# Kernel optimization log

Measured on AMD Instinct MI355X. Metric: run time of the kernel, lower is better.

The kernel has to match this reference:

```python
import jax, jax.numpy as jnp
import numpy as np

VOCAB = 256; EMB = 384; D_MODEL = 512; D_INNER = 1024; D_STATE = 16
D_CONV = 4; DT_RANK = 32; NL = 8; B = 2; L = 2048

def silu(x):
    return x * jax.nn.sigmoid(x)

def layernorm(x, g, b):
    mu = x.mean(-1, keepdims=True)
    v = ((x - mu) ** 2).mean(-1, keepdims=True)
    return (x - mu) / jnp.sqrt(v + 1e-5) * g + b

def conv1d_same(x, w, b, pad):
    # x: (B, C, L), w: (O, I, K)
    out = jax.lax.conv_general_dilated(x, w, (1,), [(pad, pad)],
                                       dimension_numbers=('NCH', 'OIH', 'NCH'))
    return out + b[None, :, None]

def mamba_layer(x, in_w, cw, cb, xp_w, dt_w, dt_b, A_log, Dp, out_w):
    # x: (B, L, D_MODEL)
    xz = x @ in_w.T                      # (B, L, 2*D_INNER)
    xi, z = xz[..., :D_INNER], xz[..., D_INNER:]
    # causal depthwise conv over time
    xi_t = xi.transpose(0, 2, 1)         # (B, D_INNER, L)
    xc = jax.lax.conv_general_dilated(xi_t, cw[:, None, :], (1,), [(D_CONV - 1, 0)],
                                      dimension_numbers=('NCH', 'OIH', 'NCH'),
                                      feature_group_count=D_INNER)
    xc = silu(xc + cb[None, :, None]).transpose(0, 2, 1)   # (B, L, D_INNER)
    dbc = xc @ xp_w.T                    # (B, L, DT_RANK + 2*D_STATE)
    dt = jax.nn.softplus(dbc[..., :DT_RANK] @ dt_w.T + dt_b)   # (B, L, D_INNER)
    Bm = dbc[..., DT_RANK:DT_RANK + D_STATE]                    # (B, L, D_STATE)
    Cm = dbc[..., DT_RANK + D_STATE:]                           # (B, L, D_STATE)
    A = -jnp.exp(A_log)                                         # (D_INNER, D_STATE)
    dA = jnp.exp(dt[..., None] * A)                             # (B, L, D_INNER, D_STATE)
    dBx = (dt * xc)[..., None] * Bm[:, :, None, :]              # (B, L, D_INNER, D_STATE)

    def step(h, inp):
        a, bx, c = inp
        h = a * h + bx                                          # (B, D_INNER, D_STATE)
        return h, jnp.einsum('bds,bs->bd', h, c)

    h0 = jnp.zeros((x.shape[0], D_INNER, D_STATE), x.dtype)
    _, ys = jax.lax.scan(step, h0, (dA.transpose(1, 0, 2, 3),
                                    dBx.transpose(1, 0, 2, 3),
                                    Cm.transpose(1, 0, 2)))
    y = ys.transpose(1, 0, 2) + Dp * xc                         # (B, L, D_INNER)
    y = y * silu(z)
    return y @ out_w.T

def setup_inputs() -> dict:
    key = jax.random.key(0)
    ks = jax.random.split(key, 24)
    s = 0.02
    inp = {
        'tokens': jax.random.randint(ks[0], (B, L), 0, VOCAB),
        'emb': jax.random.normal(ks[1], (VOCAB, EMB)) * s,
        'conv1_w': jax.random.normal(ks[2], (512, EMB, 5)) * s,
        'conv1_b': jnp.zeros((512,)),
        'ln1_g': jnp.ones((512,)), 'ln1_b': jnp.zeros((512,)),
        'conv2_w': jax.random.normal(ks[3], (512, 512, 3)) * s,
        'conv2_b': jnp.zeros((512,)),
        'ln2_g': jnp.ones((512,)), 'ln2_b': jnp.zeros((512,)),
        'pos_emb': jax.random.normal(ks[4], (L, D_MODEL)) * s,
        'in_proj_w': jax.random.normal(ks[5], (NL, 2 * D_INNER, D_MODEL)) * s,
        'conv_w': jax.random.normal(ks[6], (NL, D_INNER, D_CONV)) * s,
        'conv_b': jnp.zeros((NL, D_INNER)),
        'x_proj_w': jax.random.normal(ks[7], (NL, DT_RANK + 2 * D_STATE, D_INNER)) * s,
        'dt_proj_w': jax.random.normal(ks[8], (NL, D_INNER, DT_RANK)) * s,
        'dt_proj_b': jnp.full((NL, D_INNER), -4.0),
        'A_log': jnp.log(jnp.tile(jnp.arange(1, D_STATE + 1, dtype=jnp.float32),
                                  (NL, D_INNER, 1))),
        'D': jnp.ones((NL, D_INNER)),
        'out_proj_w': jax.random.normal(ks[9], (NL, D_MODEL, D_INNER)) * s,
        'fc_w': jax.random.normal(ks[10], (VOCAB, D_MODEL)) * s,
        'fc_b': jnp.zeros((VOCAB,)),
    }
    return inp

def reference(tokens, emb, conv1_w, conv1_b, ln1_g, ln1_b, conv2_w, conv2_b,
              ln2_g, ln2_b, pos_emb, in_proj_w, conv_w, conv_b, x_proj_w,
              dt_proj_w, dt_proj_b, A_log, D, out_proj_w, fc_w, fc_b):
    x = emb[tokens]                                   # (B, L, EMB)
    # CNN frontend (GELU + channel LayerNorm, dropout=0 in eval)
    x = x.transpose(0, 2, 1)
    x = jax.nn.gelu(conv1d_same(x, conv1_w, conv1_b, 2), approximate=False)
    x = layernorm(x.transpose(0, 2, 1), ln1_g, ln1_b).transpose(0, 2, 1)
    x = jax.nn.gelu(conv1d_same(x, conv2_w, conv2_b, 1), approximate=False)
    x = layernorm(x.transpose(0, 2, 1), ln2_g, ln2_b)  # (B, L, 512)
    x = x + pos_emb[None, :x.shape[1]]
    for i in range(NL):
        x = mamba_layer(x, in_proj_w[i], conv_w[i], conv_b[i], x_proj_w[i],
                        dt_proj_w[i], dt_proj_b[i], A_log[i], D[i], out_proj_w[i])
    rep = x[:, -1, :]
    return rep @ fc_w.T + fc_b
```

## Files before the change

kernel.cpp:

```cpp
#include <hip/hip_runtime.h>
#include <hip/hip_bf16.h>
#include <math.h>

#define VOCABN 256
#define EMBN   384
#define DM     512
#define DI     1024
#define DSTATE 16
#define DCONVN 4
#define DTRANK 32
#define NLAYER 8
#define BBATCH 2
#define LSEQ   2048
#define MROWS  (BBATCH*LSEQ)
#define SCHUNK 32
#define NCHUNK (LSEQ/SCHUNK)

typedef short s8v  __attribute__((ext_vector_type(8)));
typedef float f32x4 __attribute__((ext_vector_type(4)));

__device__ __forceinline__ ushort f2bf(float f) {
    uint u = __float_as_uint(f);
    return (ushort)((u + 0x7fffu + ((u >> 16) & 1u)) >> 16);
}
__device__ __forceinline__ float bf2f(ushort h) {
    return __uint_as_float((uint)h << 16);
}
__device__ __forceinline__ uint packbf(float f) {
    ushort h = f2bf(f);
    ushort l = f2bf(f - bf2f(h));
    return ((uint)h << 16) | (uint)l;
}
__device__ __forceinline__ void unp4(uint4 p, ushort* hdst, ushort* ldst) {
    ushort4 h, l;
    h.x = (ushort)(p.x >> 16); l.x = (ushort)(p.x & 0xffffu);
    h.y = (ushort)(p.y >> 16); l.y = (ushort)(p.y & 0xffffu);
    h.z = (ushort)(p.z >> 16); l.z = (ushort)(p.z & 0xffffu);
    h.w = (ushort)(p.w >> 16); l.w = (ushort)(p.w & 0xffffu);
    *(ushort4*)hdst = h; *(ushort4*)ldst = l;
}

__global__ void pack4_kernel(const float* __restrict__ a, int na,
                             const float* __restrict__ b, int nb,
                             const float* __restrict__ c, int nc,
                             const float* __restrict__ d, int nd,
                             uint* __restrict__ pa, uint* __restrict__ pb,
                             uint* __restrict__ pc, uint* __restrict__ pd) {
    int i = blockIdx.x * 256 + threadIdx.x;
    if (i < na) pa[i] = packbf(a[i]);
    else if (i < na + nb) pb[i - na] = packbf(b[i - na]);
    else if (i < na + nb + nc) pc[i - na - nb] = packbf(c[i - na - nb]);
    else if (i < na + nb + nc + nd) pd[i - na - nb - nc] = packbf(d[i - na - nb - nc]);
}

template<int CI, int CK>
__global__ void pack_convw_kernel(const float* __restrict__ w, uint* __restrict__ pw) {
    int idx = blockIdx.x * 256 + threadIdx.x;
    if (idx >= 512 * CI * CK) return;
    int k  = idx % CK;
    int ci = (idx / CK) % CI;
    int co = idx / (CK * CI);
    pw[((size_t)(k * 512) + co) * CI + ci] = packbf(w[idx]);
}

__global__ void embed_kernel(const int* __restrict__ tok, const float* __restrict__ emb,
                             uint* __restrict__ px0) {
    int idx = blockIdx.x * 256 + threadIdx.x;
    int c = idx % EMBN;
    int t = idx / EMBN;
    px0[idx] = packbf(emb[tok[t] * EMBN + c]);
}

__device__ __forceinline__ float gelu_exact(float x) {
    return 0.5f * x * (1.f + erff(x * 0.70710678118654752f));
}

template<int CI, int CK, int PAD>
__global__ __launch_bounds__(256) void conv_mfma_kernel(
    const uint* __restrict__ PA, const uint* __restrict__ PW,
    const float* __restrict__ bias, float* __restrict__ out)
{
    constexpr int ROWS = 64 + CK - 1;
    const int t0  = blockIdx.x * 64;
    const int co0 = blockIdx.y * 32;
    const int tid = threadIdx.x;
    const int wid = tid >> 6, lane = tid & 63;
    const int rb = (wid >> 1) * 32;
    const int cb = (wid & 1) * 16;
    const int lr = lane & 15, lk = (lane >> 4) * 8;
    const int bstart = (t0 / LSEQ) * LSEQ;

    __shared__ alignas(16) ushort Ah[ROWS][40], Al[ROWS][40];
    __shared__ alignas(16) ushort Bh[CK][32][40], Bl[CK][32][40];

    f32x4 acc[2];
#pragma unroll
    for (int m = 0; m < 2; m++) acc[m] = (f32x4){0.f, 0.f, 0.f, 0.f};

    for (int ci0 = 0; ci0 < CI; ci0 += 32) {
        __syncthreads();
        for (int idx = tid; idx < ROWS * 8; idx += 256) {
            int r = idx >> 3, c4 = (idx & 7) * 4;
            int g = t0 - PAD + r;
            uint4 v = make_uint4(0u, 0u, 0u, 0u);
            if (g >= bstart && g < bstart + LSEQ)
                v = *(const uint4*)&PA[(size_t)g * CI + ci0 + c4];
            unp4(v, &Ah[r][c4], &Al[r][c4]);
        }
        for (int idx = tid; idx < CK * 32 * 8; idx += 256) {
            int k = idx >> 8;
            int r = (idx >> 3) & 31;
            int c4 = (idx & 7) * 4;
            uint4 v = *(const uint4*)&PW[((size_t)(k * 512) + co0 + r) * CI + ci0 + c4];
            unp4(v, &Bh[k][r][c4], &Bl[k][r][c4]);
        }
        __syncthreads();

#pragma unroll
        for (int k = 0; k < CK; k++) {
            s8v ah[2], al[2], bh, bl;
#pragma unroll
            for (int m = 0; m < 2; m++) {
                ah[m] = *(const s8v*)&Ah[rb + m * 16 + lr + k][lk];
                al[m] = *(const s8v*)&Al[rb + m * 16 + lr + k][lk];
            }
            bh = *(const s8v*)&Bh[k][cb + lr][lk];
            bl = *(const s8v*)&Bl[k][cb + lr][lk];
#pragma unroll
            for (int m = 0; m < 2; m++) {
                acc[m] = __builtin_amdgcn_mfma_f32_16x16x32_bf16(ah[m], bh, acc[m], 0, 0, 0);
                acc[m] = __builtin_amdgcn_mfma_f32_16x16x32_bf16(ah[m], bl, acc[m], 0, 0, 0);
                acc[m] = __builtin_amdgcn_mfma_f32_16x16x32_bf16(al[m], bh, acc[m], 0, 0, 0);
            }
        }
    }

    int gcol = co0 + cb + lr;
    float bv = bias[gcol];
#pragma unroll
    for (int m = 0; m < 2; m++) {
#pragma unroll
        for (int r = 0; r < 4; r++) {
            int grow = t0 + rb + m * 16 + (lane >> 4) * 4 + r;
            out[(size_t)grow * 512 + gcol] = gelu_exact(acc[m][r] + bv);
        }
    }
}

template<bool ADDPOS, bool PACK>
__global__ __launch_bounds__(256) void ln_kernel(
    const float* __restrict__ in, const float* __restrict__ g, const float* __restrict__ bb,
    const float* __restrict__ pos, float* __restrict__ out, uint* __restrict__ pout)
{
    int row  = blockIdx.x * 4 + (threadIdx.x >> 6);
    int lane = threadIdx.x & 63;
    const float* xr = in + (size_t)row * DM;
    float v[8];
    float s = 0.f;
#pragma unroll
    for (int i = 0; i < 8; i++) { v[i] = xr[lane + i * 64]; s += v[i]; }
#pragma unroll
    for (int o = 32; o >= 1; o >>= 1) s += __shfl_xor(s, o);
    float mu = s * (1.f / 512.f);
    float var = 0.f;
#pragma unroll
    for (int i = 0; i < 8; i++) { float d = v[i] - mu; var = fmaf(d, d, var); }
#pragma unroll
    for (int o = 32; o >= 1; o >>= 1) var += __shfl_xor(var, o);
    var *= (1.f / 512.f);
    float rstd = rsqrtf(var + 1e-5f);
    int t = row & (LSEQ - 1);
#pragma unroll
    for (int i = 0; i < 8; i++) {
        int c = lane + i * 64;
        float o = (v[i] - mu) * rstd * g[c] + bb[c];
        if (ADDPOS) o += pos[t * DM + c];
        if (PACK) pout[(size_t)row * DM + c] = packbf(o);
        else      out [(size_t)row * DM + c] = o;
    }
}

template<int BM, int BN, int WM, int WN, int EPI>
__global__ __launch_bounds__(256) void gemm_mfma_p(
    const uint* __restrict__ PA, int lda,
    const uint* __restrict__ PW,
    const float* __restrict__ bias,
    float* __restrict__ C, uint* __restrict__ PC, int N, int K)
{
    constexpr int MR = BM / WM / 16;
    constexpr int NR = BN / WN / 16;
    constexpr int NLOAD = (BM + BN) * 8 / 256;
    const int m0 = blockIdx.x * BM;
    const int n0 = blockIdx.y * BN;
    const int tid = threadIdx.x;
    const int wid = tid >> 6;
    const int lane = tid & 63;
    const int rb = (wid / WN) * (BM / WM);
    const int cb = (wid % WN) * (BN / WN);
    const int lr = lane & 15;
    const int lk = (lane >> 4) * 8;

    __shared__ alignas(16) ushort Ah[BM][40], Al[BM][40];
    __shared__ alignas(16) ushort Bh[BN][40], Bl[BN][40];

    f32x4 acc[MR][NR];
#pragma unroll
    for (int m = 0; m < MR; m++)
#pragma unroll
        for (int n = 0; n < NR; n++) acc[m][n] = (f32x4){0.f, 0.f, 0.f, 0.f};

    for (int k0 = 0; k0 < K; k0 += 32) {
        uint4 v[NLOAD];
#pragma unroll
        for (int i = 0; i < NLOAD; i++) {
            int idx = tid + i * 256;
            int row = idx >> 3, c4 = (idx & 7) * 4;
            v[i] = (row < BM)
                 ? *(const uint4*)&PA[(size_t)(m0 + row) * lda + k0 + c4]
                 : *(const uint4*)&PW[(size_t)(n0 + row - BM) * K + k0 + c4];
        }
        __syncthreads();
#pragma unroll
        for (int i = 0; i < NLOAD; i++) {
            int idx = tid + i * 256;
            int row = idx >> 3, c4 = (idx & 7) * 4;
            if (row < BM) unp4(v[i], &Ah[row][c4], &Al[row][c4]);
            else          unp4(v[i], &Bh[row - BM][c4], &Bl[row - BM][c4]);
        }
        __syncthreads();

        s8v ah[MR], al[MR], bh[NR], bl[NR];
#pragma unroll
        for (int m = 0; m < MR; m++) {
            ah[m] = *(const s8v*)&Ah[rb + m * 16 + lr][lk];
            al[m] = *(const s8v*)&Al[rb + m * 16 + lr][lk];
        }
#pragma unroll
        for (int n = 0; n < NR; n++) {
            bh[n] = *(const s8v*)&Bh[cb + n * 16 + lr][lk];
            bl[n] = *(const s8v*)&Bl[cb + n * 16 + lr][lk];
        }
#pragma unroll
        for (int m = 0; m < MR; m++)
#pragma unroll
            for (int n = 0; n < NR; n++) {
                acc[m][n] = __builtin_amdgcn_mfma_f32_16x16x32_bf16(ah[m], bh[n], acc[m][n], 0, 0, 0);
                acc[m][n] = __builtin_amdgcn_mfma_f32_16x16x32_bf16(ah[m], bl[n], acc[m][n], 0, 0, 0);
                acc[m][n] = __builtin_amdgcn_mfma_f32_16x16x32_bf16(al[m], bh[n], acc[m][n], 0, 0, 0);
            }
    }

#pragma unroll
    for (int m = 0; m < MR; m++)
#pragma unroll
        for (int n = 0; n < NR; n++) {
#pragma unroll
            for (int r = 0; r < 4; r++) {
                int grow = m0 + rb + m * 16 + (lane >> 4) * 4 + r;
                int gcol = n0 + cb + n * 16 + lr;
                float v = acc[m][n][r];
                if (EPI == 3) {
                    v += bias[gcol];
                    v = fmaxf(v, 0.f) + log1pf(expf(-fabsf(v)));
                }
                C[(size_t)grow * N + gcol] = v;
                if (EPI == 2) PC[(size_t)grow * N + gcol] = packbf(v);
            }
        }
}

__global__ void dwconv_silu_kernel(const float* __restrict__ xz, const float* __restrict__ cw,
                                   const float* __restrict__ cb, float* __restrict__ xc,
                                   uint* __restrict__ pxc) {
    int idx = blockIdx.x * 256 + threadIdx.x;
    int d = idx & (DI - 1);
    int r = idx >> 10;
    int tl = r & (LSEQ - 1);
    float acc = cb[d];
#pragma unroll
    for (int k = 0; k < DCONVN; k++) {
        int ts = tl - 3 + k;
        if (ts >= 0) acc = fmaf(xz[(size_t)(r - 3 + k) * (2 * DI) + d], cw[d * DCONVN + k], acc);
    }
    float sig = 1.f / (1.f + expf(-acc));
    float v = acc * sig;
    xc[idx] = v;
    pxc[idx] = packbf(v);
}

__global__ __launch_bounds__(256) void scan_local_kernel(
    const float* __restrict__ dt, const float* __restrict__ xc,
    const float* __restrict__ dbc, const float* __restrict__ A_log,
    float* __restrict__ S, float* __restrict__ P)
{
    const int sg = threadIdx.x & 3;
    const int dl = threadIdx.x >> 2;
    const int dq = blockIdx.x & 15;
    const int c  = (blockIdx.x >> 4) & (NCHUNK - 1);
    const int b  = blockIdx.x / (16 * NCHUNK);
    const int d  = dq * 64 + dl;

    float4 alog = *(const float4*)&A_log[d * DSTATE + sg * 4];
    float Av[4];
    Av[0] = -expf(alog.x) * 1.44269504f;
    Av[1] = -expf(alog.y) * 1.44269504f;
    Av[2] = -expf(alog.z) * 1.44269504f;
    Av[3] = -expf(alog.w) * 1.44269504f;

    float h[4] = {0.f, 0.f, 0.f, 0.f};
    float sumdt = 0.f;
    const int rowbase = b * LSEQ + c * SCHUNK;

#pragma unroll 4
    for (int t = 0; t < SCHUNK; t++) {
        int r = rowbase + t;
        float dtv = dt[(size_t)r * DI + d];
        float xcv = xc[(size_t)r * DI + d];
        float4 Bv = *(const float4*)&dbc[(size_t)r * 64 + DTRANK + sg * 4];
        float dx = dtv * xcv;
        h[0] = fmaf(exp2f(dtv * Av[0]), h[0], dx * Bv.x);
        h[1] = fmaf(exp2f(dtv * Av[1]), h[1], dx * Bv.y);
        h[2] = fmaf(exp2f(dtv * Av[2]), h[2], dx * Bv.z);
        h[3] = fmaf(exp2f(dtv * Av[3]), h[3], dx * Bv.w);
        sumdt += dtv;
    }
    size_t off = ((size_t)(b * NCHUNK + c) * DI + d) * DSTATE + sg * 4;
    *(float4*)&S[off] = make_float4(h[0], h[1], h[2], h[3]);
    *(float4*)&P[off] = make_float4(exp2f(Av[0] * sumdt), exp2f(Av[1] * sumdt),
                                    exp2f(Av[2] * sumdt), exp2f(Av[3] * sumdt));
}

__global__ __launch_bounds__(256) void scan_combine_kernel(
    const float* __restrict__ S, const float* __restrict__ P, float* __restrict__ H)
{
    int idx = blockIdx.x * 256 + threadIdx.x;
    int b = idx >> 14;
    int rem = idx & 16383;
    float h = 0.f;
#pragma unroll
    for (int c = 0; c < NCHUNK; c++) {
        size_t off = ((size_t)(b * NCHUNK + c) * DI) * DSTATE + rem;
        H[off] = h;
        h = fmaf(P[off], h, S[off]);
    }
}

__global__ __launch_bounds__(256) void scan_out_kernel(
    const float* __restrict__ dt, const float* __restrict__ xc,
    const float* __restrict__ dbc, const float* __restrict__ xz,
    const float* __restrict__ A_log, const float* __restrict__ Dp,
    const float* __restrict__ H, uint* __restrict__ py)
{
    const int sg = threadIdx.x & 3;
    const int dl = threadIdx.x >> 2;
    const int dq = blockIdx.x & 15;
    const int c  = (blockIdx.x >> 4) & (NCHUNK - 1);
    const int b  = blockIdx.x / (16 * NCHUNK);
    const int d  = dq * 64 + dl;

    float4 alog = *(const float4*)&A_log[d * DSTATE + sg * 4];
    float Av[4];
    Av[0] = -expf(alog.x) * 1.44269504f;
    Av[1] = -expf(alog.y) * 1.44269504f;
    Av[2] = -expf(alog.z) * 1.44269504f;
    Av[3] = -expf(alog.w) * 1.44269504f;
    float Dval = Dp[d];

    float4 hv = *(const float4*)&H[((size_t)(b * NCHUNK + c) * DI + d) * DSTATE + sg * 4];
    float h[4] = {hv.x, hv.y, hv.z, hv.w};
    const int rowbase = b * LSEQ + c * SCHUNK;

#pragma unroll 2
    for (int t = 0; t < SCHUNK; t++) {
        int r = rowbase + t;
        float dtv = dt[(size_t)r * DI + d];
        float xcv = xc[(size_t)r * DI + d];
        float4 Bv = *(const float4*)&dbc[(size_t)r * 64 + DTRANK + sg * 4];
        float4 Cv = *(const float4*)&dbc[(size_t)r * 64 + DTRANK + DSTATE + sg * 4];
        float dx = dtv * xcv;
        h[0] = fmaf(exp2f(dtv * Av[0]), h[0], dx * Bv.x);
        h[1] = fmaf(exp2f(dtv * Av[1]), h[1], dx * Bv.y);
        h[2] = fmaf(exp2f(dtv * Av[2]), h[2], dx * Bv.z);
        h[3] = fmaf(exp2f(dtv * Av[3]), h[3], dx * Bv.w);
        float p = h[0] * Cv.x;
        p = fmaf(h[1], Cv.y, p);
        p = fmaf(h[2], Cv.z, p);
        p = fmaf(h[3], Cv.w, p);
        p += __shfl_xor(p, 1);
        p += __shfl_xor(p, 2);
        if (sg == 0) {
            float zv = xz[(size_t)r * (2 * DI) + DI + d];
            float zsig = 1.f / (1.f + exp2f(-zv * 1.44269504f));
            py[(size_t)r * DI + d] = packbf((p + Dval * xcv) * (zv * zsig));
        }
    }
}

__global__ void fc_kernel(const float* __restrict__ x, const float* __restrict__ fcw,
                          const float* __restrict__ fcb, float* __restrict__ out) {
    int b = blockIdx.x;
    int v = threadIdx.x;
    __shared__ float rep[DM];
    const float* xr = x + (size_t)(b * LSEQ + LSEQ - 1) * DM;
    for (int i = threadIdx.x; i < DM; i += 256) rep[i] = xr[i];
    __syncthreads();
    float acc = fcb[v];
    for (int k = 0; k < DM; k++) acc = fmaf(rep[k], fcw[v * DM + k], acc);
    out[b * VOCABN + v] = acc;
}

extern "C" void kernel_launch(void* const* d_in, const int* in_sizes, int n_in,
                              void* d_out, int out_size, void* d_ws, size_t ws_size,
                              hipStream_t stream) {
    const int*   tokens    = (const int*)  d_in[0];
    const float* emb       = (const float*)d_in[1];
    const float* conv1_w   = (const float*)d_in[2];
    const float* conv1_b   = (const float*)d_in[3];
    const float* ln1_g     = (const float*)d_in[4];
    const float* ln1_b     = (const float*)d_in[5];
    const float* conv2_w   = (const float*)d_in[6];
    const float* conv2_b   = (const float*)d_in[7];
    const float* ln2_g     = (const float*)d_in[8];
    const float* ln2_b     = (const float*)d_in[9];
    const float* pos_emb   = (const float*)d_in[10];
    const float* in_proj_w = (const float*)d_in[11];
    const float* conv_w    = (const float*)d_in[12];
    const float* conv_b    = (const float*)d_in[13];
    const float* x_proj_w  = (const float*)d_in[14];
    const float* dt_proj_w = (const float*)d_in[15];
    const float* dt_proj_b = (const float*)d_in[16];
    const float* A_log     = (const float*)d_in[17];
    const float* Dp_all    = (const float*)d_in[18];
    const float* out_proj_w= (const float*)d_in[19];
    const float* fc_w      = (const float*)d_in[20];
    const float* fc_b      = (const float*)d_in[21];

    float* ws = (float*)d_ws;
    float* X    = ws;
    float* T1   = X   + 2097152;
    float* XZ   = T1  + 2097152;
    float* XC   = XZ  + 8388608;
    float* DT   = XC  + 4194304;
    uint*  PY   = (uint*)(DT + 4194304);
    float* DBC  = (float*)PY + 4194304;
    uint*  PX   = (uint*)(DBC + 262144);
    uint*  PXC  = PX  + 2097152;
    uint*  PWIN = PXC + 4194304;
    uint*  PWOUT= PWIN + 1048576;
    uint*  PWX  = PWOUT + 524288;
    uint*  PWDT = PWX + 65536;
    uint*  PDBC = PWDT + 32768;
    uint*  PX0  = (uint*)XZ;
    uint*  PWC1 = (uint*)XC;
    uint*  PWC2 = (uint*)XC + 983040;
    uint*  PB   = (uint*)DT;
    float* SCN_S = T1;
    float* SCN_P = (float*)PXC;
    float* SCN_H = (float*)PXC + 2097152;

    pack_convw_kernel<EMBN, 5><<<(512 * EMBN * 5 + 255) / 256, 256, 0, stream>>>(conv1_w, PWC1);
    pack_convw_kernel<DM,   3><<<(512 * DM   * 3 + 255) / 256, 256, 0, stream>>>(conv2_w, PWC2);
    embed_kernel<<<(MROWS * EMBN) / 256, 256, 0, stream>>>(tokens, emb, PX0);
    conv_mfma_kernel<EMBN, 5, 2><<<dim3(MROWS / 64, 16), 256, 0, stream>>>(PX0, PWC1, conv1_b, T1);
    ln_kernel<false, true><<<MROWS / 4, 256, 0, stream>>>(T1, ln1_g, ln1_b, nullptr, nullptr, PB);
    conv_mfma_kernel<DM, 3, 1><<<dim3(MROWS / 64, 16), 256, 0, stream>>>(PB, PWC2, conv2_b, T1);
    ln_kernel<true, true><<<MROWS / 4, 256, 0, stream>>>(T1, ln2_g, ln2_b, pos_emb, nullptr, PX);

    const int NPACK = 2 * DI * DM + DM * DI + 64 * DI + DI * DTRANK;
    for (int l = 0; l < NLAYER; l++) {
        pack4_kernel<<<(NPACK + 255) / 256, 256, 0, stream>>>(
            in_proj_w + (size_t)l * 2 * DI * DM, 2 * DI * DM,
            out_proj_w + (size_t)l * DM * DI, DM * DI,
            x_proj_w + (size_t)l * 64 * DI, 64 * DI,
            dt_proj_w + (size_t)l * DI * DTRANK, DI * DTRANK,
            PWIN, PWOUT, PWX, PWDT);
        gemm_mfma_p<64, 128, 1, 4, 0><<<dim3(MROWS / 64, (2 * DI) / 128), 256, 0, stream>>>(
            PX, DM, PWIN, nullptr, XZ, nullptr, 2 * DI, DM);
        dwconv_silu_kernel<<<(MROWS * DI) / 256, 256, 0, stream>>>(
            XZ, conv_w + (size_t)l * DI * DCONVN, conv_b + (size_t)l * DI, XC, PXC);
        gemm_mfma_p<64, 64, 2, 2, 2><<<dim3(MROWS / 64, 1), 256, 0, stream>>>(
            PXC, DI, PWX, nullptr, DBC, PDBC, 64, DI);
        gemm_mfma_p<64, 64, 2, 2, 3><<<dim3(MROWS / 64, DI / 64), 256, 0, stream>>>(
            PDBC, 64, PWDT, dt_proj_b + (size_t)l * DI, DT, nullptr, DI, DTRANK);
        scan_local_kernel<<<16 * NCHUNK * BBATCH, 256, 0, stream>>>(
            DT, XC, DBC, A_log + (size_t)l * DI * DSTATE, SCN_S, SCN_P);
        scan_combine_kernel<<<(BBATCH * DI * DSTATE) / 256, 256, 0, stream>>>(
            SCN_S, SCN_P, SCN_H);
        scan_out_kernel<<<16 * NCHUNK * BBATCH, 256, 0, stream>>>(
            DT, XC, DBC, XZ, A_log + (size_t)l * DI * DSTATE, Dp_all + (size_t)l * DI,
            SCN_H, PY);
        gemm_mfma_p<64, 64, 2, 2, 2><<<dim3(MROWS / 64, DM / 64), 256, 0, stream>>>(
            PY, DI, PWOUT, nullptr, X, PX, DM, DI);
    }

    fc_kernel<<<BBATCH, 256, 0, stream>>>(X, fc_w, fc_b, (float*)d_out);
}
```

Before: 1.868 ms.

## Restructure chunked scan: compute local outputs in first pass, apply state correction elementwise

The two sequential per-chunk scan passes become one. The forward pass now computes the chunk-local output and the cumulative dt in the same loop that produces the chunk end-states. A new elementwise kernel then adds the carried-in state contribution using exp(A*cumdt)*H*C and applies the z gate. A_log is turned into A*log2e once inside the packing kernel, so the scan kernels no longer call exp on it. This removes a second sequential recurrence over each chunk, at the cost of extra fp32 round trips through memory and 16 exp2 calls per output element in the correction kernel.

New measurement: 1.924 ms. 1.03x slower.

```diff
diff --git a/kernel.cpp b/kernel.cpp
--- a/kernel.cpp
+++ b/kernel.cpp
@@ -40,17 +40,23 @@
     *(ushort4*)hdst = h; *(ushort4*)ldst = l;
 }
 
-__global__ void pack4_kernel(const float* __restrict__ a, int na,
+__global__ void pack5_kernel(const float* __restrict__ a, int na,
                              const float* __restrict__ b, int nb,
                              const float* __restrict__ c, int nc,
                              const float* __restrict__ d, int nd,
+                             const float* __restrict__ alog, int ne,
                              uint* __restrict__ pa, uint* __restrict__ pb,
-                             uint* __restrict__ pc, uint* __restrict__ pd) {
+                             uint* __restrict__ pc, uint* __restrict__ pd,
+                             float* __restrict__ av) {
     int i = blockIdx.x * 256 + threadIdx.x;
     if (i < na) pa[i] = packbf(a[i]);
     else if (i < na + nb) pb[i - na] = packbf(b[i - na]);
     else if (i < na + nb + nc) pc[i - na - nb] = packbf(c[i - na - nb]);
     else if (i < na + nb + nc + nd) pd[i - na - nb - nc] = packbf(d[i - na - nb - nc]);
+    else if (i < na + nb + nc + nd + ne) {
+        int j = i - na - nb - nc - nd;
+        av[j] = -expf(alog[j]) * 1.44269504f;
+    }
 }
 
 template<int CI, int CK>
@@ -263,8 +269,10 @@
                     v += bias[gcol];
                     v = fmaxf(v, 0.f) + log1pf(expf(-fabsf(v)));
                 }
-                C[(size_t)grow * N + gcol] = v;
-                if (EPI == 2) PC[(size_t)grow * N + gcol] = packbf(v);
+                if (EPI == 0 || EPI == 2 || EPI == 3)
+                    C[(size_t)grow * N + gcol] = v;
+                if (EPI == 2)
+                    PC[(size_t)grow * N + gcol] = packbf(v);
             }
         }
 }
@@ -288,10 +296,14 @@
     pxc[idx] = packbf(v);
 }
 
-__global__ __launch_bounds__(256) void scan_local_kernel(
-    const float* __restrict__ dt, const float* __restrict__ xc,
-    const float* __restrict__ dbc, const float* __restrict__ A_log,
-    float* __restrict__ S, float* __restrict__ P)
+__global__ __launch_bounds__(256) void scan_fwd_kernel(
+    float* dtbuf,
+    const float* __restrict__ xc,
+    const float* __restrict__ dbc,
+    const float* __restrict__ AV,
+    const float* __restrict__ Dp,
+    float* __restrict__ S, float* __restrict__ P,
+    float* __restrict__ ylocal)
 {
     const int sg = threadIdx.x & 3;
     const int dl = threadIdx.x >> 2;
@@ -300,83 +312,22 @@
     const int b  = blockIdx.x / (16 * NCHUNK);
     const int d  = dq * 64 + dl;
 
-    float4 alog = *(const float4*)&A_log[d * DSTATE + sg * 4];
-    float Av[4];
-    Av[0] = -expf(alog.x) * 1.44269504f;
-    Av[1] = -expf(alog.y) * 1.44269504f;
-    Av[2] = -expf(alog.z) * 1.44269504f;
-    Av[3] = -expf(alog.w) * 1.44269504f;
+    float4 av = *(const float4*)&AV[d * DSTATE + sg * 4];
+    float Av[4] = {av.x, av.y, av.z, av.w};
+    float Dval = Dp[d];
 
     float h[4] = {0.f, 0.f, 0.f, 0.f};
     float sumdt = 0.f;
     const int rowbase = b * LSEQ + c * SCHUNK;
 
-#pragma unroll 4
-    for (int t = 0; t < SCHUNK; t++) {
-        int r = rowbase + t;
-        float dtv = dt[(size_t)r * DI + d];
-        float xcv = xc[(size_t)r * DI + d];
-        float4 Bv = *(const float4*)&dbc[(size_t)r * 64 + DTRANK + sg * 4];
-        float dx = dtv * xcv;
-        h[0] = fmaf(exp2f(dtv * Av[0]), h[0], dx * Bv.x);
-        h[1] = fmaf(exp2f(dtv * Av[1]), h[1], dx * Bv.y);
-        h[2] = fmaf(exp2f(dtv * Av[2]), h[2], dx * Bv.z);
-        h[3] = fmaf(exp2f(dtv * Av[3]), h[3], dx * Bv.w);
-        sumdt += dtv;
-    }
-    size_t off = ((size_t)(b * NCHUNK + c) * DI + d) * DSTATE + sg * 4;
-    *(float4*)&S[off] = make_float4(h[0], h[1], h[2], h[3]);
-    *(float4*)&P[off] = make_float4(exp2f(Av[0] * sumdt), exp2f(Av[1] * sumdt),
-                                    exp2f(Av[2] * sumdt), exp2f(Av[3] * sumdt));
-}
-
-__global__ __launch_bounds__(256) void scan_combine_kernel(
-    const float* __restrict__ S, const float* __restrict__ P, float* __restrict__ H)
-{
-    int idx = blockIdx.x * 256 + threadIdx.x;
-    int b = idx >> 14;
-    int rem = idx & 16383;
-    float h = 0.f;
-#pragma unroll
-    for (int c = 0; c < NCHUNK; c++) {
-        size_t off = ((size_t)(b * NCHUNK + c) * DI) * DSTATE + rem;
-        H[off] = h;
-        h = fmaf(P[off], h, S[off]);
-    }
-}
-
-__global__ __launch_bounds__(256) void scan_out_kernel(
-    const float* __restrict__ dt, const float* __restrict__ xc,
-    const float* __restrict__ dbc, const float* __restrict__ xz,
-    const float* __restrict__ A_log, const float* __restrict__ Dp,
-    const float* __restrict__ H, uint* __restrict__ py)
-{
-    const int sg = threadIdx.x & 3;
-    const int dl = threadIdx.x >> 2;
-    const int dq = blockIdx.x & 15;
-    const int c  = (blockIdx.x >> 4) & (NCHUNK - 1);
-    const int b  = blockIdx.x / (16 * NCHUNK);
-    const int d  = dq * 64 + dl;
-
-    float4 alog = *(const float4*)&A_log[d * DSTATE + sg * 4];
-    float Av[4];
-    Av[0] = -expf(alog.x) * 1.44269504f;
-    Av[1] = -expf(alog.y) * 1.44269504f;
-    Av[2] = -expf(alog.z) * 1.44269504f;
-    Av[3] = -expf(alog.w) * 1.44269504f;
-    float Dval = Dp[d];
-
-    float4 hv = *(const float4*)&H[((size_t)(b * NCHUNK + c) * DI + d) * DSTATE + sg * 4];
-    float h[4] = {hv.x, hv.y, hv.z, hv.w};
-    const int rowbase = b * LSEQ + c * SCHUNK;
-
 #pragma unroll 2
     for (int t = 0; t < SCHUNK; t++) {
-        int r = rowbase + t;
-        float dtv = dt[(size_t)r * DI + d];
-        float xcv = xc[(size_t)r * DI + d];
-        float4 Bv = *(const float4*)&dbc[(size_t)r * 64 + DTRANK + sg * 4];
-        float4 Cv = *(const float4*)&dbc[(size_t)r * 64 + DTRANK + DSTATE + sg * 4];
+        size_t off = (size_t)(rowbase + t) * DI + d;
+        float dtv = dtbuf[off];
+        float xcv = xc[off];
+        float4 Bv = *(const float4*)&dbc[(size_t)(rowbase + t) * 64 + DTRANK + sg * 4];
+        float4 Cv = *(const float4*)&dbc[(size_t)(rowbase + t) * 64 + DTRANK + DSTATE + sg * 4];
+        sumdt += dtv;
         float dx = dtv * xcv;
         h[0] = fmaf(exp2f(dtv * Av[0]), h[0], dx * Bv.x);
         h[1] = fmaf(exp2f(dtv * Av[1]), h[1], dx * Bv.y);
@@ -389,11 +340,66 @@
         p += __shfl_xor(p, 1);
         p += __shfl_xor(p, 2);
         if (sg == 0) {
-            float zv = xz[(size_t)r * (2 * DI) + DI + d];
-            float zsig = 1.f / (1.f + exp2f(-zv * 1.44269504f));
-            py[(size_t)r * DI + d] = packbf((p + Dval * xcv) * (zv * zsig));
-        }
-    }
+            ylocal[off] = p + Dval * xcv;
+            dtbuf[off] = sumdt;
+        }
+    }
+    size_t soff = ((size_t)(b * NCHUNK + c) * DI + d) * DSTATE + sg * 4;
+    *(float4*)&S[soff] = make_float4(h[0], h[1], h[2], h[3]);
+    *(float4*)&P[soff] = make_float4(exp2f(Av[0] * sumdt), exp2f(Av[1] * sumdt),
+                                     exp2f(Av[2] * sumdt), exp2f(Av[3] * sumdt));
+}
+
+__global__ __launch_bounds__(256) void scan_combine_kernel(
+    const float* __restrict__ S, const float* __restrict__ P, float* __restrict__ H)
+{
+    int idx = blockIdx.x * 256 + threadIdx.x;
+    int b = idx >> 14;
+    int rem = idx & 16383;
+    float h = 0.f;
+#pragma unroll
+    for (int c = 0; c < NCHUNK; c++) {
+        size_t off = ((size_t)(b * NCHUNK + c) * DI) * DSTATE + rem;
+        H[off] = h;
+        h = fmaf(P[off], h, S[off]);
+    }
+}
+
+__global__ __launch_bounds__(256) void scan_corr_kernel(
+    const float* __restrict__ cumdt,
+    const float* __restrict__ dbc,
+    const float* __restrict__ xz,
+    const float* __restrict__ AV,
+    const float* __restrict__ H,
+    uint* __restrict__ py)
+{
+    int idx = blockIdx.x * 256 + threadIdx.x;
+    int d = idx & (DI - 1);
+    int r = idx >> 10;
+    int t = r & (LSEQ - 1);
+    int b = r >> 11;
+    int c = t / SCHUNK;
+
+    float cd = cumdt[idx];
+    float yl = __uint_as_float(py[idx]);
+    float zv = xz[(size_t)r * (2 * DI) + DI + d];
+    const float* Hp = &H[((size_t)(b * NCHUNK + c) * DI + d) * DSTATE];
+    const float* Cp = &dbc[(size_t)r * 64 + DTRANK + DSTATE];
+    const float* Ap = &AV[d * DSTATE];
+
+    float corr = 0.f;
+#pragma unroll
+    for (int s = 0; s < DSTATE; s += 4) {
+        float4 Hv = *(const float4*)&Hp[s];
+        float4 Cv = *(const float4*)&Cp[s];
+        float4 Avv = *(const float4*)&Ap[s];
+        corr = fmaf(Cv.x * exp2f(Avv.x * cd), Hv.x, corr);
+        corr = fmaf(Cv.y * exp2f(Avv.y * cd), Hv.y, corr);
+        corr = fmaf(Cv.z * exp2f(Avv.z * cd), Hv.z, corr);
+        corr = fmaf(Cv.w * exp2f(Avv.w * cd), Hv.w, corr);
+    }
+    float zsig = 1.f / (1.f + exp2f(-zv * 1.44269504f));
+    py[idx] = packbf((yl + corr) * (zv * zsig));
 }
 
 __global__ void fc_kernel(const float* __restrict__ x, const float* __restrict__ fcw,
@@ -450,6 +456,7 @@
     uint*  PWX  = PWOUT + 524288;
     uint*  PWDT = PWX + 65536;
     uint*  PDBC = PWDT + 32768;
+    float* AVB  = (float*)(PDBC + 262144);
     uint*  PX0  = (uint*)XZ;
     uint*  PWC1 = (uint*)XC;
     uint*  PWC2 = (uint*)XC + 983040;
@@ -466,14 +473,15 @@
     conv_mfma_kernel<DM, 3, 1><<<dim3(MROWS / 64, 16), 256, 0, stream>>>(PB, PWC2, conv2_b, T1);
     ln_kernel<true, true><<<MROWS / 4, 256, 0, stream>>>(T1, ln2_g, ln2_b, pos_emb, nullptr, PX);
 
-    const int NPACK = 2 * DI * DM + DM * DI + 64 * DI + DI * DTRANK;
+    const int NPACK = 2 * DI * DM + DM * DI + 64 * DI + DI * DTRANK + DI * DSTATE;
     for (int l = 0; l < NLAYER; l++) {
-        pack4_kernel<<<(NPACK + 255) / 256, 256, 0, stream>>>(
+        pack5_kernel<<<(NPACK + 255) / 256, 256, 0, stream>>>(
             in_proj_w + (size_t)l * 2 * DI * DM, 2 * DI * DM,
             out_proj_w + (size_t)l * DM * DI, DM * DI,
             x_proj_w + (size_t)l * 64 * DI, 64 * DI,
             dt_proj_w + (size_t)l * DI * DTRANK, DI * DTRANK,
-            PWIN, PWOUT, PWX, PWDT);
+            A_log + (size_t)l * DI * DSTATE, DI * DSTATE,
+            PWIN, PWOUT, PWX, PWDT, AVB);
         gemm_mfma_p<64, 128, 1, 4, 0><<<dim3(MROWS / 64, (2 * DI) / 128), 256, 0, stream>>>(
             PX, DM, PWIN, nullptr, XZ, nullptr, 2 * DI, DM);
         dwconv_silu_kernel<<<(MROWS * DI) / 256, 256, 0, stream>>>(
@@ -482,13 +490,12 @@
             PXC, DI, PWX, nullptr, DBC, PDBC, 64, DI);
         gemm_mfma_p<64, 64, 2, 2, 3><<<dim3(MROWS / 64, DI / 64), 256, 0, stream>>>(
             PDBC, 64, PWDT, dt_proj_b + (size_t)l * DI, DT, nullptr, DI, DTRANK);
-        scan_local_kernel<<<16 * NCHUNK * BBATCH, 256, 0, stream>>>(
-            DT, XC, DBC, A_log + (size_t)l * DI * DSTATE, SCN_S, SCN_P);
+        scan_fwd_kernel<<<16 * NCHUNK * BBATCH, 256, 0, stream>>>(
+            DT, XC, DBC, AVB, Dp_all + (size_t)l * DI, SCN_S, SCN_P, (float*)PY);
         scan_combine_kernel<<<(BBATCH * DI * DSTATE) / 256, 256, 0, stream>>>(
             SCN_S, SCN_P, SCN_H);
-        scan_out_kernel<<<16 * NCHUNK * BBATCH, 256, 0, stream>>>(
-            DT, XC, DBC, XZ, A_log + (size_t)l * DI * DSTATE, Dp_all + (size_t)l * DI,
-            SCN_H, PY);
+        scan_corr_kernel<<<(MROWS * DI) / 256, 256, 0, stream>>>(
+            DT, DBC, XZ, AVB, SCN_H, PY);
         gemm_mfma_p<64, 64, 2, 2, 2><<<dim3(MROWS / 64, DM / 64), 256, 0, stream>>>(
             PY, DI, PWOUT, nullptr, X, PX, DM, DI);
     }
```
